# Kernel optimization log

Hardware: AMD Instinct MI355X
Metric: run time of the kernel (lower is better)

The kernel has to match this reference:

```python
import jax, jax.numpy as jnp
import numpy as np

N, D, R, E, ED = 50000, 128, 8, 800000, 32
BN_EPS = 1e-5


def _bn(x, g, b):
    # training-mode BatchNorm1d: biased batch stats over axis 0
    m = jnp.mean(x, axis=0)
    v = jnp.var(x, axis=0)
    return (x - m) * jax.lax.rsqrt(v + BN_EPS) * g + b


def _aggregate(x, node_in, nor, ew_norm, edge_feature, We, be):
    # fused: ew * x[node_in] + ew * edge_linear(edge_feature), single scatter-add
    msg = ew_norm[:, None] * (x[node_in] + edge_feature @ We + be)  # [E, D]
    return jax.ops.segment_sum(msg, nor, num_segments=N * R)  # [N*R, D]


def _forward(x, node_in, node_out, relation, edge_weight, edge_feature,
             l1_Wlin, l1_blin, l1_Wself, l1_bself, l1_Wedge, l1_bedge, l1_g, l1_b,
             l2_Wlin, l2_blin, l2_Wself, l2_bself, l2_Wedge, l2_bedge, l2_g, l2_b):
    nor = node_out * R + relation  # [E], expanded destination index
    deg = jax.ops.segment_sum(edge_weight, nor, num_segments=N * R)
    ew = edge_weight / deg[nor]  # degree-normalized edge weights
    # layer 1: relationalGraphConv (update viewed as [N, R*D])
    u1 = _aggregate(x, node_in, nor, ew, edge_feature, l1_Wedge, l1_bedge)
    u1 = u1.reshape(N, R * D)
    h = u1 @ l1_Wlin + l1_blin + x @ l1_Wself + l1_bself
    h = jax.nn.relu(_bn(h, l1_g, l1_b))
    # layer 2: relationalGraph (update permuted to [R*N, D])
    u2 = _aggregate(h, node_in, nor, ew, edge_feature, l2_Wedge, l2_bedge)
    u2 = u2.reshape(N, R, D).transpose(1, 0, 2).reshape(R * N, D)
    h_rep = jnp.tile(h, (R, 1))  # input.repeat(num_relation, 1)
    o = u2 @ l2_Wlin + l2_blin + h_rep @ l2_Wself + l2_bself
    o = jax.nn.relu(_bn(o, l2_g, l2_b))
    return o.reshape(R, N, D)


def setup_inputs() -> dict:
    key = jax.random.key(0)
    ks = jax.random.split(key, 12)
    s_in = 1.0 / np.sqrt(D)
    s_lin1 = 1.0 / np.sqrt(R * D)
    s_e = 1.0 / np.sqrt(ED)
    return {
        "x": jax.random.normal(ks[0], (N, D), jnp.float32),
        "node_in": jax.random.randint(ks[1], (E,), 0, N),
        "node_out": jax.random.randint(ks[2], (E,), 0, N),
        "relation": jax.random.randint(ks[3], (E,), 0, R),
        "edge_weight": jnp.ones((E,), jnp.float32),
        "edge_feature": jax.random.normal(ks[4], (E, ED), jnp.float32),
        "l1_Wlin": jax.random.normal(ks[5], (R * D, D), jnp.float32) * s_lin1,
        "l1_blin": jnp.zeros((D,), jnp.float32),
        "l1_Wself": jax.random.normal(ks[6], (D, D), jnp.float32) * s_in,
        "l1_bself": jnp.zeros((D,), jnp.float32),
        "l1_Wedge": jax.random.normal(ks[7], (ED, D), jnp.float32) * s_e,
        "l1_bedge": jnp.zeros((D,), jnp.float32),
        "l1_g": jnp.ones((D,), jnp.float32),
        "l1_b": jnp.zeros((D,), jnp.float32),
        "l2_Wlin": jax.random.normal(ks[8], (D, D), jnp.float32) * s_in,
        "l2_blin": jnp.zeros((D,), jnp.float32),
        "l2_Wself": jax.random.normal(ks[9], (D, D), jnp.float32) * s_in,
        "l2_bself": jnp.zeros((D,), jnp.float32),
        "l2_Wedge": jax.random.normal(ks[10], (ED, D), jnp.float32) * s_e,
        "l2_bedge": jnp.zeros((D,), jnp.float32),
        "l2_g": jnp.ones((D,), jnp.float32),
        "l2_b": jnp.zeros((D,), jnp.float32),
    }


def reference(x, node_in, node_out, relation, edge_weight, edge_feature,
              l1_Wlin, l1_blin, l1_Wself, l1_bself, l1_Wedge, l1_bedge, l1_g, l1_b,
              l2_Wlin, l2_blin, l2_Wself, l2_bself, l2_Wedge, l2_bedge, l2_g, l2_b):
    return _forward(x, node_in, node_out, relation, edge_weight, edge_feature,
                    l1_Wlin, l1_blin, l1_Wself, l1_bself, l1_Wedge, l1_bedge, l1_g, l1_b,
                    l2_Wlin, l2_blin, l2_Wself, l2_bself, l2_Wedge, l2_bedge, l2_g, l2_b)
```

## Files before the change

### kernel.cpp

```cpp
#include <hip/hip_runtime.h>
#include <hip/hip_bf16.h>

#define Nn 50000
#define Dd 128
#define Rr 8
#define Ee 800000
#define EDd 32
#define NR (Nn * Rr)
#define BN_EPS 1e-5f
#define NREP 16

typedef __attribute__((ext_vector_type(8))) short short8;
typedef __attribute__((ext_vector_type(4))) float floatx4;
typedef unsigned short u16;

__device__ inline float bf2f(u16 u) {
    unsigned int x = ((unsigned int)u) << 16;
    return __uint_as_float(x);
}
__device__ inline u16 f2bf(float f) {
    __hip_bfloat16 h = __float2bfloat16(f);
    return *(u16*)&h;
}
__device__ inline u16 f2h(float f) {
    _Float16 h = (_Float16)f;
    return *(u16*)&h;
}
__device__ inline float h2f(u16 u) {
    _Float16 h = *(_Float16*)&u;
    return (float)h;
}

__global__ __launch_bounds__(256) void k_deg(const int* __restrict__ node_out,
                                             const int* __restrict__ relation,
                                             const float* __restrict__ w_in,
                                             float* __restrict__ deg,
                                             int* __restrict__ cnt) {
    int e = blockIdx.x * 256 + threadIdx.x;
    if (e >= Ee) return;
    int idx = node_out[e] * Rr + relation[e];
    unsafeAtomicAdd(deg + idx, w_in[e]);
    atomicAdd(cnt + idx, 1);
}

__global__ __launch_bounds__(256) void k_scan1(const int* __restrict__ cnt,
                                               int* __restrict__ base,
                                               int* __restrict__ partials) {
    __shared__ int sd[256];
    int b0 = blockIdx.x * 1024;
    int t = threadIdx.x;
    int v[4], s = 0;
    #pragma unroll
    for (int j = 0; j < 4; ++j) {
        int idx = b0 + t * 4 + j;
        v[j] = (idx < NR) ? cnt[idx] : 0;
        s += v[j];
    }
    sd[t] = s;
    __syncthreads();
    for (int off = 1; off < 256; off <<= 1) {
        int xv = (t >= off) ? sd[t - off] : 0;
        __syncthreads();
        sd[t] += xv;
        __syncthreads();
    }
    int excl = sd[t] - s;
    if (t == 255) partials[blockIdx.x] = sd[255];
    int run = excl;
    #pragma unroll
    for (int j = 0; j < 4; ++j) {
        int idx = b0 + t * 4 + j;
        if (idx < NR) base[idx] = run;
        run += v[j];
    }
}

__global__ __launch_bounds__(512) void k_scan2(int* __restrict__ partials, int n) {
    __shared__ int sd[512];
    int t = threadIdx.x;
    int own = (t < n) ? partials[t] : 0;
    sd[t] = own;
    __syncthreads();
    for (int off = 1; off < 512; off <<= 1) {
        int xv = (t >= off) ? sd[t - off] : 0;
        __syncthreads();
        sd[t] += xv;
        __syncthreads();
    }
    if (t < n) partials[t] = sd[t] - own;
}

__global__ __launch_bounds__(256) void k_scan3(int* __restrict__ base,
                                               const int* __restrict__ partials) {
    int b0 = blockIdx.x * 1024;
    int add = partials[blockIdx.x];
    int t = threadIdx.x;
    #pragma unroll
    for (int j = 0; j < 4; ++j) {
        int idx = b0 + t * 4 + j;
        if (idx < NR) base[idx] += add;
    }
}

__global__ __launch_bounds__(256) void k_scatter(const int* __restrict__ node_in,
                                                 const int* __restrict__ node_out,
                                                 const int* __restrict__ relation,
                                                 const float* __restrict__ w_in,
                                                 const float* __restrict__ deg,
                                                 int* __restrict__ base,
                                                 int4* __restrict__ recs) {
    int e = blockIdx.x * 256 + threadIdx.x;
    if (e >= Ee) return;
    int idx = node_out[e] * Rr + relation[e];
    int pos = atomicAdd(base + idx, 1);
    int4 r;
    r.x = node_in[e];
    r.y = __float_as_int(w_in[e] / deg[idx]);
    r.z = e;
    r.w = 0;
    recs[pos] = r;
}

__global__ __launch_bounds__(256) void k_cvt(const float* __restrict__ src,
                                             u16* __restrict__ dst, long n) {
    long i = ((long)blockIdx.x * 256 + threadIdx.x) * 4;
    if (i >= n) return;
    float4 v = *(const float4*)(src + i);
    ushort4 o;
    o.x = f2bf(v.x); o.y = f2bf(v.y); o.z = f2bf(v.z); o.w = f2bf(v.w);
    *(ushort4*)(dst + i) = o;
}

__global__ __launch_bounds__(256) void k_prepB(const float* __restrict__ W1,
                                               const float* __restrict__ Ws1,
                                               const float* __restrict__ W2,
                                               const float* __restrict__ Ws2,
                                               u16* __restrict__ Bt) {
    int idx = blockIdx.x * 256 + threadIdx.x;
    if (idx >= 11 * 16384) return;
    int p = idx >> 14;
    int n = (idx >> 7) & 127;
    int k = idx & 127;
    float v;
    if (p < 8)       v = W1[((p << 7) + k) * 128 + n];
    else if (p == 8) v = Ws1[k * 128 + n];
    else if (p == 9) v = W2[k * 128 + n];
    else             v = Ws2[k * 128 + n];
    Bt[((long)p << 14) + n * 128 + k] = f2bf(v);
}

__global__ __launch_bounds__(256) void k_prepWef1(const float* __restrict__ We,
                                                  const float* __restrict__ be,
                                                  const float* __restrict__ Wlin,
                                                  u16* __restrict__ out) {
    int idx = blockIdx.x * 256 + threadIdx.x;
    if (idx >= 3 * 16384) return;
    int n = (idx >> 7) & 127;
    int k = idx & 127;
    int kk = (idx >> 14) * 128 + k;
    int p = kk / 40, j = kk % 40;
    float acc = 0.f;
    if (kk < 320 && j < 33) {
        for (int t = 0; t < 128; ++t) {
            float m = (j < 32) ? We[j * 128 + t] : be[t];
            acc = fmaf(m, Wlin[(p * 128 + t) * 128 + n], acc);
        }
    }
    out[idx] = f2bf(acc);
}

__global__ __launch_bounds__(256) void k_prepWef2(const float* __restrict__ We,
                                                  const float* __restrict__ be,
                                                  const float* __restrict__ Wlin,
                                                  u16* __restrict__ out) {
    int idx = blockIdx.x * 256 + threadIdx.x;
    if (idx >= 8192) return;
    int n = idx >> 6;
    int k = idx & 63;
    float acc = 0.f;
    if (k < 33) {
        for (int t = 0; t < 128; ++t) {
            float m = (k < 32) ? We[k * 128 + t] : be[t];
            acc = fmaf(m, Wlin[t * 128 + n], acc);
        }
    }
    out[idx] = f2bf(acc);
}

__global__ __launch_bounds__(256) void k_agg1(const u16* __restrict__ src,
                                              const int* __restrict__ base_end,
                                              const int* __restrict__ cnt,
                                              const int4* __restrict__ recs,
                                              const float* __restrict__ ef,
                                              u16* __restrict__ u,
                                              u16* __restrict__ aggef_x) {
    int gid = threadIdx.x >> 4;
    int gl = threadIdx.x & 15;
    int gl8 = gl * 8, gl2 = gl * 2;
    for (long d = (long)blockIdx.x * 16 + gid; d < NR; d += (long)gridDim.x * 16) {
        int end = base_end[d];
        int c = cnt[d];
        int e = end - c;
        float a[8] = {0.f, 0.f, 0.f, 0.f, 0.f, 0.f, 0.f, 0.f};
        float e0 = 0.f, e1 = 0.f;
        for (; e + 4 <= end; e += 4) {
            int4 r0 = recs[e],     r1 = recs[e + 1];
            int4 r2 = recs[e + 2], r3 = recs[e + 3];
            short8 x0 = *(const short8*)(src + (long)r0.x * Dd + gl8);
            short8 x1 = *(const short8*)(src + (long)r1.x * Dd + gl8);
            short8 x2 = *(const short8*)(src + (long)r2.x * Dd + gl8);
            short8 x3 = *(const short8*)(src + (long)r3.x * Dd + gl8);
            float2 f0 = *(const float2*)(ef + (long)r0.z * EDd + gl2);
            float2 f1 = *(const float2*)(ef + (long)r1.z * EDd + gl2);
            float2 f2 = *(const float2*)(ef + (long)r2.z * EDd + gl2);
            float2 f3 = *(const float2*)(ef + (long)r3.z * EDd + gl2);
            float w0 = __int_as_float(r0.y), w1 = __int_as_float(r1.y);
            float w2 = __int_as_float(r2.y), w3 = __int_as_float(r3.y);
            #pragma unroll
            for (int j = 0; j < 8; ++j) {
                a[j] = fmaf(w0, bf2f((u16)x0[j]), a[j]);
                a[j] = fmaf(w1, bf2f((u16)x1[j]), a[j]);
                a[j] = fmaf(w2, bf2f((u16)x2[j]), a[j]);
                a[j] = fmaf(w3, bf2f((u16)x3[j]), a[j]);
            }
            e0 = fmaf(w0, f0.x, e0); e0 = fmaf(w1, f1.x, e0);
            e0 = fmaf(w2, f2.x, e0); e0 = fmaf(w3, f3.x, e0);
            e1 = fmaf(w0, f0.y, e1); e1 = fmaf(w1, f1.y, e1);
            e1 = fmaf(w2, f2.y, e1); e1 = fmaf(w3, f3.y, e1);
        }
        if (e + 2 <= end) {
            int4 r0 = recs[e], r1 = recs[e + 1];
            short8 x0 = *(const short8*)(src + (long)r0.x * Dd + gl8);
            short8 x1 = *(const short8*)(src + (long)r1.x * Dd + gl8);
            float2 f0 = *(const float2*)(ef + (long)r0.z * EDd + gl2);
            float2 f1 = *(const float2*)(ef + (long)r1.z * EDd + gl2);
            float w0 = __int_as_float(r0.y), w1 = __int_as_float(r1.y);
            #pragma unroll
            for (int j = 0; j < 8; ++j) {
                a[j] = fmaf(w0, bf2f((u16)x0[j]), a[j]);
                a[j] = fmaf(w1, bf2f((u16)x1[j]), a[j]);
            }
            e0 = fmaf(w0, f0.x, e0); e0 = fmaf(w1, f1.x, e0);
            e1 = fmaf(w0, f0.y, e1); e1 = fmaf(w1, f1.y, e1);
            e += 2;
        }
        if (e < end) {
            int4 r0 = recs[e];
            float w0 = __int_as_float(r0.y);
            short8 x0 = *(const short8*)(src + (long)r0.x * Dd + gl8);
            float2 f0 = *(const float2*)(ef + (long)r0.z * EDd + gl2);
            #pragma unroll
            for (int j = 0; j < 8; ++j)
                a[j] = fmaf(w0, bf2f((u16)x0[j]), a[j]);
            e0 = fmaf(w0, f0.x, e0);
            e1 = fmaf(w0, f0.y, e1);
        }
        short8 o;
        #pragma unroll
        for (int j = 0; j < 8; ++j) o[j] = (short)f2bf(a[j]);
        *(short8*)(u + d * Dd + gl8) = o;
        ushort2 ev;
        ev.x = f2bf(e0);
        ev.y = f2bf(e1);
        *(ushort2*)(aggef_x + d * 40 + gl2) = ev;
        if (gl < 4) {
            ushort2 t;
            t.x = (gl == 0 && c > 0) ? (u16)0x3F80 : (u16)0;
            t.y = 0;
            *(ushort2*)(aggef_x + d * 40 + 32 + gl2) = t;
        }
    }
}

template <int NK>
__device__ __forceinline__ void l1_panel2(const u16* __restrict__ Ap,
                                          const long* __restrict__ aoff,
                                          const u16* __restrict__ Bp, int br0, int br1,
                                          int kq8, floatx4 (&acc)[2][2]) {
    short8 a[2][NK], b[2][NK];
    #pragma unroll
    for (int kk = 0; kk < NK; ++kk) {
        #pragma unroll
        for (int ti = 0; ti < 2; ++ti)
            a[ti][kk] = *(const short8*)(Ap + aoff[ti] + kk * 32 + kq8);
        b[0][kk] = *(const short8*)(Bp + (long)br0 * 128 + kk * 32 + kq8);
        b[1][kk] = *(const short8*)(Bp + (long)br1 * 128 + kk * 32 + kq8);
    }
    #pragma unroll
    for (int kk = 0; kk < NK; ++kk)
        #pragma unroll
        for (int ti = 0; ti < 2; ++ti)
            #pragma unroll
            for (int tj = 0; tj < 2; ++tj)
                acc[ti][tj] = __builtin_amdgcn_mfma_f32_16x16x32_bf16(
                    a[ti][kk], b[tj][kk], acc[ti][tj], 0, 0, 0);
}

template <int NK>
__device__ __forceinline__ void l2_panel(const u16* __restrict__ Ap,
                                         const long* __restrict__ aoff,
                                         const u16* __restrict__ Bp, long bstride,
                                         const int* __restrict__ brow, int koff,
                                         int kq8, floatx4 (&acc)[4][4]) {
    short8 a[4][NK], b[4][NK];
    #pragma unroll
    for (int kk = 0; kk < NK; ++kk) {
        #pragma unroll
        for (int ti = 0; ti < 4; ++ti)
            a[ti][kk] = *(const short8*)(Ap + aoff[ti] + koff + kk * 32 + kq8);
        #pragma unroll
        for (int tj = 0; tj < 4; ++tj)
            b[tj][kk] = *(const short8*)(Bp + (long)brow[tj] * bstride + koff + kk * 32 + kq8);
    }
    #pragma unroll
    for (int kk = 0; kk < NK; ++kk)
        #pragma unroll
        for (int ti = 0; ti < 4; ++ti)
            #pragma unroll
            for (int tj = 0; tj < 4; ++tj)
                acc[ti][tj] = __builtin_amdgcn_mfma_f32_16x16x32_bf16(
                    a[ti][kk], b[tj][kk], acc[ti][tj], 0, 0, 0);
}

__global__ __launch_bounds__(256) void k_gemm_l1(const u16* __restrict__ U,
                                                 const u16* __restrict__ Xb,
                                                 const u16* __restrict__ Bt,
                                                 const u16* __restrict__ Wef,
                                                 const u16* __restrict__ Ax,
                                                 u16* __restrict__ Hpre,
                                                 float* __restrict__ stats) {
    const int tid = threadIdx.x;
    const int wave = tid >> 6, lane = tid & 63;
    const int l15 = lane & 15, kq = lane >> 4;
    const int kq8 = kq * 8;
    const int n0w = wave * 32;
    const int m0 = blockIdx.x * 32;
    const int br0 = n0w + l15, br1 = n0w + 16 + l15;

    floatx4 acc[2][2];
    #pragma unroll
    for (int i = 0; i < 2; ++i)
        #pragma unroll
        for (int j = 0; j < 2; ++j)
            acc[i][j] = (floatx4){0.f, 0.f, 0.f, 0.f};

    long mb[2];
    int mrow[2];
    #pragma unroll
    for (int ti = 0; ti < 2; ++ti) {
        int m = m0 + ti * 16 + l15;
        if (m >= Nn) m = Nn - 1;
        mrow[ti] = m;
        mb[ti] = (long)m * 1024;
    }

    long aoff[2];
    #pragma unroll
    for (int p = 0; p < 8; ++p) {
        #pragma unroll
        for (int ti = 0; ti < 2; ++ti) aoff[ti] = mb[ti] + p * 128;
        l1_panel2<4>(U, aoff, Bt + ((long)p << 14), br0, br1, kq8, acc);
    }
    #pragma unroll
    for (int ti = 0; ti < 2; ++ti) aoff[ti] = (long)mrow[ti] * 128;
    l1_panel2<4>(Xb, aoff, Bt + (8L << 14), br0, br1, kq8, acc);
    #pragma unroll
    for (int q = 0; q < 2; ++q) {
        #pragma unroll
        for (int ti = 0; ti < 2; ++ti) aoff[ti] = (long)mrow[ti] * 320 + q * 128;
        l1_panel2<4>(Ax, aoff, Wef + ((long)q << 14), br0, br1, kq8, acc);
    }
    #pragma unroll
    for (int ti = 0; ti < 2; ++ti) aoff[ti] = (long)mrow[ti] * 320 + 256;
    l1_panel2<2>(Ax, aoff, Wef + (2L << 14), br0, br1, kq8, acc);

    float cs[2] = {0.f, 0.f}, cq[2] = {0.f, 0.f};
    #pragma unroll
    for (int ti = 0; ti < 2; ++ti) {
        #pragma unroll
        for (int r = 0; r < 4; ++r) {
            int m = m0 + ti * 16 + kq * 4 + r;
            if (m < Nn) {
                #pragma unroll
                for (int tj = 0; tj < 2; ++tj) {
                    float v = acc[ti][tj][r];
                    int col = n0w + tj * 16 + l15;
                    Hpre[(long)m * Dd + col] = f2bf(v);
                    cs[tj] += v;
                    cq[tj] = fmaf(v, v, cq[tj]);
                }
            }
        }
    }
    #pragma unroll
    for (int tj = 0; tj < 2; ++tj) {
        cs[tj] += __shfl_xor(cs[tj], 16, 64);
        cs[tj] += __shfl_xor(cs[tj], 32, 64);
        cq[tj] += __shfl_xor(cq[tj], 16, 64);
        cq[tj] += __shfl_xor(cq[tj], 32, 64);
    }
    if (kq == 0) {
        int rep = blockIdx.x & (NREP - 1);
        #pragma unroll
        for (int tj = 0; tj < 2; ++tj) {
            int col = n0w + tj * 16 + l15;
            unsafeAtomicAdd(stats + rep * 256 + col, cs[tj]);
            unsafeAtomicAdd(stats + rep * 256 + 128 + col, cq[tj]);
        }
    }
}

__global__ __launch_bounds__(256) void k_gemm_ht(const u16* __restrict__ H,
                                                 const u16* __restrict__ Bt,
                                                 u16* __restrict__ ht,
                                                 u16* __restrict__ hsp) {
    const int tid = threadIdx.x;
    const int wave = tid >> 6, lane = tid & 63;
    const int l15 = lane & 15, kq = lane >> 4;
    const int kq8 = kq * 8;
    const int n0w = wave * 32;
    const int m0 = blockIdx.x * 32;
    const int br0 = n0w + l15, br1 = n0w + 16 + l15;

    long aoff[2];
    #pragma unroll
    for (int ti = 0; ti < 2; ++ti) {
        int m = m0 + ti * 16 + l15;
        if (m >= Nn) m = Nn - 1;
        aoff[ti] = (long)m * 128;
    }

    floatx4 acc0[2][2], acc1[2][2];
    #pragma unroll
    for (int i = 0; i < 2; ++i)
        #pragma unroll
        for (int j = 0; j < 2; ++j) {
            acc0[i][j] = (floatx4){0.f, 0.f, 0.f, 0.f};
            acc1[i][j] = (floatx4){0.f, 0.f, 0.f, 0.f};
        }

    short8 a[2][4], b0[2][4], b1[2][4];
    const u16* Bp0 = Bt + (9L << 14);
    const u16* Bp1 = Bt + (10L << 14);
    #pragma unroll
    for (int kk = 0; kk < 4; ++kk) {
        #pragma unroll
        for (int ti = 0; ti < 2; ++ti)
            a[ti][kk] = *(const short8*)(H + aoff[ti] + kk * 32 + kq8);
        b0[0][kk] = *(const short8*)(Bp0 + (long)br0 * 128 + kk * 32 + kq8);
        b0[1][kk] = *(const short8*)(Bp0 + (long)br1 * 128 + kk * 32 + kq8);
        b1[0][kk] = *(const short8*)(Bp1 + (long)br0 * 128 + kk * 32 + kq8);
        b1[1][kk] = *(const short8*)(Bp1 + (long)br1 * 128 + kk * 32 + kq8);
    }
    #pragma unroll
    for (int kk = 0; kk < 4; ++kk)
        #pragma unroll
        for (int ti = 0; ti < 2; ++ti)
            #pragma unroll
            for (int tj = 0; tj < 2; ++tj) {
                acc0[ti][tj] = __builtin_amdgcn_mfma_f32_16x16x32_bf16(
                    a[ti][kk], b0[tj][kk], acc0[ti][tj], 0, 0, 0);
                acc1[ti][tj] = __builtin_amdgcn_mfma_f32_16x16x32_bf16(
                    a[ti][kk], b1[tj][kk], acc1[ti][tj], 0, 0, 0);
            }

    #pragma unroll
    for (int ti = 0; ti < 2; ++ti) {
        #pragma unroll
        for (int r = 0; r < 4; ++r) {
            int m = m0 + ti * 16 + kq * 4 + r;
            if (m < Nn) {
                #pragma unroll
                for (int tj = 0; tj < 2; ++tj) {
                    int col = n0w + tj * 16 + l15;
                    ht[(long)m * Dd + col] = f2bf(acc0[ti][tj][r]);
                    hsp[(long)m * Dd + col] = f2bf(acc1[ti][tj][r]);
                }
            }
        }
    }
}

__global__ __launch_bounds__(256) void k_gemm_agf2(const u16* __restrict__ Ax,
                                                   const u16* __restrict__ Wef2,
                                                   u16* __restrict__ agf2) {
    const int tid = threadIdx.x;
    const int wave = tid >> 6, lane = tid & 63;
    const int l15 = lane & 15, kq = lane >> 4;
    const int kq8 = kq * 8;
    const int wm = wave & 1, wn = wave >> 1;
    const int n0w = wn * 64;
    const long m0 = (long)blockIdx.x * 128;

    int brow[4];
    #pragma unroll
    for (int tj = 0; tj < 4; ++tj) brow[tj] = n0w + tj * 16 + l15;

    floatx4 acc[4][4];
    #pragma unroll
    for (int i = 0; i < 4; ++i)
        #pragma unroll
        for (int j = 0; j < 4; ++j)
            acc[i][j] = (floatx4){0.f, 0.f, 0.f, 0.f};

    long aoffE[4];
    #pragma unroll
    for (int ti = 0; ti < 4; ++ti)
        aoffE[ti] = (m0 + wm * 64 + ti * 16 + l15) * 40L;

    l2_panel<2>(Ax, aoffE, Wef2, 64, brow, 0, kq8, acc);

    #pragma unroll
    for (int ti = 0; ti < 4; ++ti) {
        #pragma unroll
        for (int r = 0; r < 4; ++r) {
            long mm = m0 + wm * 64 + ti * 16 + kq * 4 + r;
            #pragma unroll
            for (int tj = 0; tj < 4; ++tj)
                agf2[mm * Dd + n0w + tj * 16 + l15] = f2h(acc[ti][tj][r]);
        }
    }
}

__global__ __launch_bounds__(256) void k_out(const u16* __restrict__ ht,
                                             const u16* __restrict__ hsp,
                                             const int* __restrict__ base_end,
                                             const int* __restrict__ cnt,
                                             const int4* __restrict__ recs,
                                             u16* __restrict__ pre,
                                             float* __restrict__ stats) {
    __shared__ float sd[16][256];
    int gid = threadIdx.x >> 4;
    int gl = threadIdx.x & 15;
    int gl8 = gl * 8;
    float s[8] = {0, 0, 0, 0, 0, 0, 0, 0}, q[8] = {0, 0, 0, 0, 0, 0, 0, 0};
    for (long d = (long)blockIdx.x * 16 + gid; d < NR; d += (long)gridDim.x * 16) {
        int end = base_end[d];
        int c = cnt[d];
        int e = end - c;
        long n = d >> 3;
        short8 hv = *(const short8*)(hsp + n * Dd + gl8);
        short8 gv = *(const short8*)(pre + d * Dd + gl8);
        float a[8];
        #pragma unroll
        for (int j = 0; j < 8; ++j)
            a[j] = bf2f((u16)hv[j]) + h2f((u16)gv[j]);
        for (; e + 4 <= end; e += 4) {
            int4 r0 = recs[e],     r1 = recs[e + 1];
            int4 r2 = recs[e + 2], r3 = recs[e + 3];
            short8 x0 = *(const short8*)(ht + (long)r0.x * Dd + gl8);
            short8 x1 = *(const short8*)(ht + (long)r1.x * Dd + gl8);
            short8 x2 = *(const short8*)(ht + (long)r2.x * Dd + gl8);
            short8 x3 = *(const short8*)(ht + (long)r3.x * Dd + gl8);
            float w0 = __int_as_float(r0.y), w1 = __int_as_float(r1.y);
            float w2 = __int_as_float(r2.y), w3 = __int_as_float(r3.y);
            #pragma unroll
            for (int j = 0; j < 8; ++j) {
                a[j] = fmaf(w0, bf2f((u16)x0[j]), a[j]);
                a[j] = fmaf(w1, bf2f((u16)x1[j]), a[j]);
                a[j] = fmaf(w2, bf2f((u16)x2[j]), a[j]);
                a[j] = fmaf(w3, bf2f((u16)x3[j]), a[j]);
            }
        }
        if (e + 2 <= end) {
            int4 r0 = recs[e], r1 = recs[e + 1];
            short8 x0 = *(const short8*)(ht + (long)r0.x * Dd + gl8);
            short8 x1 = *(const short8*)(ht + (long)r1.x * Dd + gl8);
            float w0 = __int_as_float(r0.y), w1 = __int_as_float(r1.y);
            #pragma unroll
            for (int j = 0; j < 8; ++j) {
                a[j] = fmaf(w0, bf2f((u16)x0[j]), a[j]);
                a[j] = fmaf(w1, bf2f((u16)x1[j]), a[j]);
            }
            e += 2;
        }
        if (e < end) {
            int4 r0 = recs[e];
            float w0 = __int_as_float(r0.y);
            short8 x0 = *(const short8*)(ht + (long)r0.x * Dd + gl8);
            #pragma unroll
            for (int j = 0; j < 8; ++j)
                a[j] = fmaf(w0, bf2f((u16)x0[j]), a[j]);
        }
        short8 o;
        #pragma unroll
        for (int j = 0; j < 8; ++j) {
            o[j] = (short)f2h(a[j]);
            s[j] += a[j];
            q[j] = fmaf(a[j], a[j], q[j]);
        }
        *(short8*)(pre + d * Dd + gl8) = o;
    }
    #pragma unroll
    for (int j = 0; j < 8; ++j) {
        sd[gid][gl8 + j] = s[j];
        sd[gid][128 + gl8 + j] = q[j];
    }
    __syncthreads();
    int t = threadIdx.x;
    float acc = 0.f;
    #pragma unroll
    for (int g = 0; g < 16; ++g) acc += sd[g][t];
    unsafeAtomicAdd(stats + (blockIdx.x & (NREP - 1)) * 256 + t, acc);
}

__global__ __launch_bounds__(256) void k_bn_apply_bf(u16* __restrict__ X,
                                                     const float* __restrict__ stats,
                                                     const float* __restrict__ g,
                                                     const float* __restrict__ b, int M) {
    int c = (threadIdx.x & 31) * 4;
    int rh = threadIdx.x >> 5;
    float invM = 1.0f / (float)M;
    float s[4] = {0, 0, 0, 0}, q[4] = {0, 0, 0, 0};
    for (int rep = 0; rep < NREP; ++rep) {
        float4 s4 = *(const float4*)(stats + rep * 256 + c);
        float4 q4 = *(const float4*)(stats + rep * 256 + 128 + c);
        s[0] += s4.x; s[1] += s4.y; s[2] += s4.z; s[3] += s4.w;
        q[0] += q4.x; q[1] += q4.y; q[2] += q4.z; q[3] += q4.w;
    }
    float4 g4 = *(const float4*)(g + c);
    float4 b4 = *(const float4*)(b + c);
    float gv[4] = {g4.x, g4.y, g4.z, g4.w};
    float bv[4] = {b4.x, b4.y, b4.z, b4.w};
    float sc[4], sh[4];
    #pragma unroll
    for (int j = 0; j < 4; ++j) {
        float m = s[j] * invM;
        sc[j] = gv[j] / sqrtf(q[j] * invM - m * m + BN_EPS);
        sh[j] = bv[j] - m * sc[j];
    }
    for (long r = blockIdx.x * 8 + rh; r < M; r += (long)gridDim.x * 8) {
        ushort4 v = *(ushort4*)(X + r * Dd + c);
        ushort4 o;
        o.x = f2bf(fmaxf(fmaf(bf2f(v.x), sc[0], sh[0]), 0.f));
        o.y = f2bf(fmaxf(fmaf(bf2f(v.y), sc[1], sh[1]), 0.f));
        o.z = f2bf(fmaxf(fmaf(bf2f(v.z), sc[2], sh[2]), 0.f));
        o.w = f2bf(fmaxf(fmaf(bf2f(v.w), sc[3], sh[3]), 0.f));
        *(ushort4*)(X + r * Dd + c) = o;
    }
}

__global__ __launch_bounds__(256) void k_bn_out(const u16* __restrict__ pre,
                                                const float* __restrict__ stats,
                                                const float* __restrict__ g,
                                                const float* __restrict__ b,
                                                float* __restrict__ out) {
    int c = (threadIdx.x & 31) * 4;
    int rh = threadIdx.x >> 5;
    const float invM = 1.0f / (float)NR;
    float s[4] = {0, 0, 0, 0}, q[4] = {0, 0, 0, 0};
    for (int rep = 0; rep < NREP; ++rep) {
        float4 s4 = *(const float4*)(stats + rep * 256 + c);
        float4 q4 = *(const float4*)(stats + rep * 256 + 128 + c);
        s[0] += s4.x; s[1] += s4.y; s[2] += s4.z; s[3] += s4.w;
        q[0] += q4.x; q[1] += q4.y; q[2] += q4.z; q[3] += q4.w;
    }
    float4 g4 = *(const float4*)(g + c);
    float4 b4 = *(const float4*)(b + c);
    float gv[4] = {g4.x, g4.y, g4.z, g4.w};
    float bv[4] = {b4.x, b4.y, b4.z, b4.w};
    float sc[4], sh[4];
    #pragma unroll
    for (int j = 0; j < 4; ++j) {
        float m = s[j] * invM;
        sc[j] = gv[j] / sqrtf(q[j] * invM - m * m + BN_EPS);
        sh[j] = bv[j] - m * sc[j];
    }
    for (int m = blockIdx.x * 8 + rh; m < NR; m += gridDim.x * 8) {
        int r = m / Nn;
        int n = m - r * Nn;
        ushort4 v = *(const ushort4*)(pre + ((long)n * 8 + r) * Dd + c);
        float4 o;
        o.x = fmaxf(fmaf(h2f(v.x), sc[0], sh[0]), 0.f);
        o.y = fmaxf(fmaf(h2f(v.y), sc[1], sh[1]), 0.f);
        o.z = fmaxf(fmaf(h2f(v.z), sc[2], sh[2]), 0.f);
        o.w = fmaxf(fmaf(h2f(v.w), sc[3], sh[3]), 0.f);
        *(float4*)(out + (long)m * Dd + c) = o;
    }
}

extern "C" void kernel_launch(void* const* d_in, const int* in_sizes, int n_in,
                              void* d_out, int out_size, void* d_ws, size_t ws_size,
                              hipStream_t stream) {
    const float* x            = (const float*)d_in[0];
    const int*   node_in      = (const int*)d_in[1];
    const int*   node_out     = (const int*)d_in[2];
    const int*   relation     = (const int*)d_in[3];
    const float* edge_weight  = (const float*)d_in[4];
    const float* edge_feature = (const float*)d_in[5];
    const float* l1_Wlin  = (const float*)d_in[6];
    const float* l1_Wself = (const float*)d_in[8];
    const float* l1_Wedge = (const float*)d_in[10];
    const float* l1_bedge = (const float*)d_in[11];
    const float* l1_g     = (const float*)d_in[12];
    const float* l1_b     = (const float*)d_in[13];
    const float* l2_Wlin  = (const float*)d_in[14];
    const float* l2_Wself = (const float*)d_in[16];
    const float* l2_Wedge = (const float*)d_in[18];
    const float* l2_bedge = (const float*)d_in[19];
    const float* l2_g     = (const float*)d_in[20];
    const float* l2_b     = (const float*)d_in[21];
    float* out = (float*)d_out;

    u16* u_bf    = (u16*)d_ws;
    u16* h       = u_bf + (long)NR * Dd;
    u16* x_bf    = h + (long)Nn * Dd;
    u16* aggef_x = x_bf + (long)Nn * Dd;
    u16* Bt      = aggef_x + (long)NR * 40 + 128;
    u16* Wef1    = Bt + 11 * 16384;
    u16* Wef2    = Wef1 + 3 * 16384;
    float* deg   = (float*)(Wef2 + 8192);
    int*   cnt   = (int*)(deg + NR);
    int*   base  = cnt + NR;
    int4*  recs  = (int4*)(base + NR);
    int*   partials = (int*)(recs + Ee);
    float* stats = (float*)(partials + 1024);
    u16* agf2 = u_bf;
    u16* ht   = x_bf;
    u16* hsp  = aggef_x;

    const int NB1 = (NR + 1023) / 1024;

    hipMemsetAsync(deg, 0, sizeof(float) * NR, stream);
    hipMemsetAsync(cnt, 0, sizeof(int) * NR, stream);
    hipMemsetAsync(stats, 0, sizeof(float) * 2 * NREP * 256, stream);
    hipMemsetAsync(aggef_x + (long)NR * 40, 0, 256, stream);
    k_deg<<<(Ee + 255) / 256, 256, 0, stream>>>(node_out, relation, edge_weight, deg, cnt);
    k_scan1<<<NB1, 256, 0, stream>>>(cnt, base, partials);
    k_scan2<<<1, 512, 0, stream>>>(partials, NB1);
    k_scan3<<<NB1, 256, 0, stream>>>(base, partials);
    k_scatter<<<(Ee + 255) / 256, 256, 0, stream>>>(node_in, node_out, relation, edge_weight,
                                                    deg, base, recs);
    k_cvt<<<((long)Nn * Dd / 4 + 255) / 256, 256, 0, stream>>>(x, x_bf, (long)Nn * Dd);
    k_prepB<<<(11 * 16384 + 255) / 256, 256, 0, stream>>>(l1_Wlin, l1_Wself, l2_Wlin, l2_Wself, Bt);
    k_prepWef1<<<(3 * 16384 + 255) / 256, 256, 0, stream>>>(l1_Wedge, l1_bedge, l1_Wlin, Wef1);
    k_prepWef2<<<32, 256, 0, stream>>>(l2_Wedge, l2_bedge, l2_Wlin, Wef2);

    k_agg1<<<4096, 256, 0, stream>>>(x_bf, base, cnt, recs, edge_feature, u_bf, aggef_x);
    k_gemm_l1<<<(Nn + 31) / 32, 256, 0, stream>>>(u_bf, x_bf, Bt, Wef1, aggef_x, h, stats);
    k_bn_apply_bf<<<512, 256, 0, stream>>>(h, stats, l1_g, l1_b, Nn);

    k_gemm_agf2<<<NR / 128, 256, 0, stream>>>(aggef_x, Wef2, agf2);
    k_gemm_ht<<<(Nn + 31) / 32, 256, 0, stream>>>(h, Bt, ht, hsp);
    k_out<<<2048, 256, 0, stream>>>(ht, hsp, base, cnt, recs, agf2, stats + NREP * 256);
    k_bn_out<<<2048, 256, 0, stream>>>(agf2, stats + NREP * 256, l2_g, l2_b, out);
}
```

Before: 892.7 us.

## Double-buffer layer-1 GEMM panels with a larger 64-row tile

The layer-1 GEMM now computes 64 rows per block instead of 32, so each B panel load is reused across four row tiles. K-panels are software-pipelined through two register buffers, and sched_barrier calls keep the next panel's loads separate from the current panel's MFMAs. Launch bounds ask for two blocks per CU. Sched barriers are also added to the layer-2 panel helper and the ht GEMM. The costs are higher register pressure and a final edge-feature panel that now loads a full 128-wide K slice where 64 was used before. That slice reads past the 320-wide row and relies on the zero-padded weights.

```diff
diff --git a/kernel.cpp b/kernel.cpp
--- a/kernel.cpp
+++ b/kernel.cpp
@@ -273,30 +273,6 @@
 }
 
 template <int NK>
-__device__ __forceinline__ void l1_panel2(const u16* __restrict__ Ap,
-                                          const long* __restrict__ aoff,
-                                          const u16* __restrict__ Bp, int br0, int br1,
-                                          int kq8, floatx4 (&acc)[2][2]) {
-    short8 a[2][NK], b[2][NK];
-    #pragma unroll
-    for (int kk = 0; kk < NK; ++kk) {
-        #pragma unroll
-        for (int ti = 0; ti < 2; ++ti)
-            a[ti][kk] = *(const short8*)(Ap + aoff[ti] + kk * 32 + kq8);
-        b[0][kk] = *(const short8*)(Bp + (long)br0 * 128 + kk * 32 + kq8);
-        b[1][kk] = *(const short8*)(Bp + (long)br1 * 128 + kk * 32 + kq8);
-    }
-    #pragma unroll
-    for (int kk = 0; kk < NK; ++kk)
-        #pragma unroll
-        for (int ti = 0; ti < 2; ++ti)
-            #pragma unroll
-            for (int tj = 0; tj < 2; ++tj)
-                acc[ti][tj] = __builtin_amdgcn_mfma_f32_16x16x32_bf16(
-                    a[ti][kk], b[tj][kk], acc[ti][tj], 0, 0, 0);
-}
-
-template <int NK>
 __device__ __forceinline__ void l2_panel(const u16* __restrict__ Ap,
                                          const long* __restrict__ aoff,
                                          const u16* __restrict__ Bp, long bstride,
@@ -312,6 +288,7 @@
         for (int tj = 0; tj < 4; ++tj)
             b[tj][kk] = *(const short8*)(Bp + (long)brow[tj] * bstride + koff + kk * 32 + kq8);
     }
+    __builtin_amdgcn_sched_barrier(0);
     #pragma unroll
     for (int kk = 0; kk < NK; ++kk)
         #pragma unroll
@@ -322,61 +299,95 @@
                     a[ti][kk], b[tj][kk], acc[ti][tj], 0, 0, 0);
 }
 
-__global__ __launch_bounds__(256) void k_gemm_l1(const u16* __restrict__ U,
-                                                 const u16* __restrict__ Xb,
-                                                 const u16* __restrict__ Bt,
-                                                 const u16* __restrict__ Wef,
-                                                 const u16* __restrict__ Ax,
-                                                 u16* __restrict__ Hpre,
-                                                 float* __restrict__ stats) {
+__global__ __launch_bounds__(256, 2) void k_gemm_l1(const u16* __restrict__ U,
+                                                    const u16* __restrict__ Xb,
+                                                    const u16* __restrict__ Bt,
+                                                    const u16* __restrict__ Wef,
+                                                    const u16* __restrict__ Ax,
+                                                    u16* __restrict__ Hpre,
+                                                    float* __restrict__ stats) {
     const int tid = threadIdx.x;
     const int wave = tid >> 6, lane = tid & 63;
     const int l15 = lane & 15, kq = lane >> 4;
     const int kq8 = kq * 8;
     const int n0w = wave * 32;
-    const int m0 = blockIdx.x * 32;
+    const int m0 = blockIdx.x * 64;
     const int br0 = n0w + l15, br1 = n0w + 16 + l15;
 
-    floatx4 acc[2][2];
-    #pragma unroll
-    for (int i = 0; i < 2; ++i)
+    floatx4 acc[4][2];
+    #pragma unroll
+    for (int i = 0; i < 4; ++i)
         #pragma unroll
         for (int j = 0; j < 2; ++j)
             acc[i][j] = (floatx4){0.f, 0.f, 0.f, 0.f};
 
-    long mb[2];
-    int mrow[2];
-    #pragma unroll
-    for (int ti = 0; ti < 2; ++ti) {
+    long mb[4];
+    int mrow[4];
+    #pragma unroll
+    for (int ti = 0; ti < 4; ++ti) {
         int m = m0 + ti * 16 + l15;
         if (m >= Nn) m = Nn - 1;
         mrow[ti] = m;
         mb[ti] = (long)m * 1024;
     }
 
-    long aoff[2];
-    #pragma unroll
-    for (int p = 0; p < 8; ++p) {
-        #pragma unroll
-        for (int ti = 0; ti < 2; ++ti) aoff[ti] = mb[ti] + p * 128;
-        l1_panel2<4>(U, aoff, Bt + ((long)p << 14), br0, br1, kq8, acc);
-    }
-    #pragma unroll
-    for (int ti = 0; ti < 2; ++ti) aoff[ti] = (long)mrow[ti] * 128;
-    l1_panel2<4>(Xb, aoff, Bt + (8L << 14), br0, br1, kq8, acc);
-    #pragma unroll
-    for (int q = 0; q < 2; ++q) {
-        #pragma unroll
-        for (int ti = 0; ti < 2; ++ti) aoff[ti] = (long)mrow[ti] * 320 + q * 128;
-        l1_panel2<4>(Ax, aoff, Wef + ((long)q << 14), br0, br1, kq8, acc);
-    }
-    #pragma unroll
-    for (int ti = 0; ti < 2; ++ti) aoff[ti] = (long)mrow[ti] * 320 + 256;
-    l1_panel2<2>(Ax, aoff, Wef + (2L << 14), br0, br1, kq8, acc);
+    auto loadPanel = [&](int p, short8 (&a)[4][4], short8 (&b)[2][4]) {
+        const u16* Ap;
+        const u16* Bp;
+        long aoff[4];
+        if (p < 8) {
+            Ap = U;
+            Bp = Bt + ((long)p << 14);
+            #pragma unroll
+            for (int ti = 0; ti < 4; ++ti) aoff[ti] = mb[ti] + p * 128;
+        } else if (p == 8) {
+            Ap = Xb;
+            Bp = Bt + (8L << 14);
+            #pragma unroll
+            for (int ti = 0; ti < 4; ++ti) aoff[ti] = (long)mrow[ti] * 128;
+        } else {
+            Ap = Ax;
+            Bp = Wef + ((long)(p - 9) << 14);
+            #pragma unroll
+            for (int ti = 0; ti < 4; ++ti) aoff[ti] = (long)mrow[ti] * 320 + (p - 9) * 128;
+        }
+        #pragma unroll
+        for (int kk = 0; kk < 4; ++kk) {
+            #pragma unroll
+            for (int ti = 0; ti < 4; ++ti)
+                a[ti][kk] = *(const short8*)(Ap + aoff[ti] + kk * 32 + kq8);
+            b[0][kk] = *(const short8*)(Bp + (long)br0 * 128 + kk * 32 + kq8);
+            b[1][kk] = *(const short8*)(Bp + (long)br1 * 128 + kk * 32 + kq8);
+        }
+    };
+    auto mmaPanel = [&](short8 (&a)[4][4], short8 (&b)[2][4]) {
+        #pragma unroll
+        for (int kk = 0; kk < 4; ++kk)
+            #pragma unroll
+            for (int ti = 0; ti < 4; ++ti)
+                #pragma unroll
+                for (int tj = 0; tj < 2; ++tj)
+                    acc[ti][tj] = __builtin_amdgcn_mfma_f32_16x16x32_bf16(
+                        a[ti][kk], b[tj][kk], acc[ti][tj], 0, 0, 0);
+    };
+
+    short8 aA[4][4], bA[2][4], aB[4][4], bB[2][4];
+    loadPanel(0, aA, bA);
+    #pragma unroll
+    for (int p = 0; p < 12; p += 2) {
+        if (p + 1 < 12) loadPanel(p + 1, aB, bB);
+        __builtin_amdgcn_sched_barrier(0);
+        mmaPanel(aA, bA);
+        __builtin_amdgcn_sched_barrier(0);
+        if (p + 2 < 12) loadPanel(p + 2, aA, bA);
+        __builtin_amdgcn_sched_barrier(0);
+        mmaPanel(aB, bB);
+        __builtin_amdgcn_sched_barrier(0);
+    }
 
     float cs[2] = {0.f, 0.f}, cq[2] = {0.f, 0.f};
     #pragma unroll
-    for (int ti = 0; ti < 2; ++ti) {
+    for (int ti = 0; ti < 4; ++ti) {
         #pragma unroll
         for (int r = 0; r < 4; ++r) {
             int m = m0 + ti * 16 + kq * 4 + r;
@@ -452,6 +463,7 @@
         b1[0][kk] = *(const short8*)(Bp1 + (long)br0 * 128 + kk * 32 + kq8);
         b1[1][kk] = *(const short8*)(Bp1 + (long)br1 * 128 + kk * 32 + kq8);
     }
+    __builtin_amdgcn_sched_barrier(0);
     #pragma unroll
     for (int kk = 0; kk < 4; ++kk)
         #pragma unroll
@@ -737,7 +749,7 @@
     k_prepWef2<<<32, 256, 0, stream>>>(l2_Wedge, l2_bedge, l2_Wlin, Wef2);
 
     k_agg1<<<4096, 256, 0, stream>>>(x_bf, base, cnt, recs, edge_feature, u_bf, aggef_x);
-    k_gemm_l1<<<(Nn + 31) / 32, 256, 0, stream>>>(u_bf, x_bf, Bt, Wef1, aggef_x, h, stats);
+    k_gemm_l1<<<(Nn + 63) / 64, 256, 0, stream>>>(u_bf, x_bf, Bt, Wef1, aggef_x, h, stats);
     k_bn_apply_bf<<<512, 256, 0, stream>>>(h, stats, l1_g, l1_b, Nn);
 
     k_gemm_agf2<<<NR / 128, 256, 0, stream>>>(aggef_x, Wef2, agf2);
```

Result: faster. 873.7 us (-2.1%).
